# Performance work log

Measured on AMD Instinct MI355X. Metric: run time of the kernel, lower is better.

The kernel has to match this reference:

```python
import jax, jax.numpy as jnp
import numpy as np

B, T, D, DI, K, M, H, HD, L, VOCAB = 8, 512, 256, 512, 4, 2, 4, 64, 2, 272


def rmsnorm(x, w, eps=1e-6):
    return x * jax.lax.rsqrt(jnp.mean(x * x, axis=-1, keepdims=True) + eps) * w


def rotate_half(x):
    x1, x2 = x[..., ::2], x[..., 1::2]
    return jnp.stack([-x2, x1], axis=-1).reshape(x.shape)


def causal_conv(x, w, b):
    # x: [B,T,C], w: [C,K] depthwise causal conv, then silu
    y = jax.lax.conv_general_dilated(
        x.transpose(0, 2, 1), w[:, None, :],
        window_strides=(1,), padding=[(K - 1, 0)],
        feature_group_count=x.shape[-1])
    return jax.nn.silu(y.transpose(0, 2, 1) + b)


def delta_memory(x, Wv, Wg, Wb, Wa, A_log, dt_bias, Wblend, Wout):
    # x: [B,T,D]; per-timestep delta-rule fast-weight update with decay + key rotation
    Bv, Tn, Dm = x.shape
    vals = (x @ Wv).reshape(Bv, Tn, M, H, HD)
    gate = jax.nn.sigmoid(x @ Wg)                                   # [B,T,H]
    beta = jax.nn.sigmoid(jnp.einsum('btd,mdh->btmh', x, Wb))       # [B,T,M,H]
    alpha = jnp.einsum('btd,mdh->btmh', x, Wa) + dt_bias            # [B,T,M,H]
    decay = jnp.exp(-jnp.exp(A_log)[None, None] * jax.nn.softplus(alpha))
    blend = jax.nn.softmax((x @ Wblend).reshape(Bv, Tn, H, M), axis=-1)
    rk0 = x.reshape(Bv, Tn, H, HD)
    rk0 = rk0 / jnp.maximum(jnp.linalg.norm(rk0, axis=-1, keepdims=True), 1e-12)
    rks = [rk0]
    for _ in range(M - 1):
        rks.append(rotate_half(rks[-1]))
    rks = jnp.stack(rks, axis=2)                                    # [B,T,M,H,d]
    wks = jnp.pad(rks[:, :-1], ((0, 0), (1, 0), (0, 0), (0, 0), (0, 0)))  # shifted keys

    def step(S, inp):
        v, wk, rk, bt, dc, bl, g = inp
        S = S * dc[..., None, None]                                  # [B,M,H,d,d]
        pred = jnp.einsum('bmhdk,bmhd->bmhk', S, wk)
        err = (v - pred) * bt[..., None]
        S = S + wk[..., None] * err[..., None, :]                    # outer-product write
        read = jnp.einsum('bmhdk,bmhd->bmhk', S, rk)
        o = jnp.einsum('bhm,bmhk->bhk', bl, read) * g[..., None]
        return S, o

    tf = lambda a: jnp.moveaxis(a, 1, 0)
    xs = (tf(vals), tf(wks), tf(rks), tf(beta), tf(decay), tf(blend), tf(gate))
    S0 = jnp.zeros((Bv, M, H, HD, HD), x.dtype)
    _, o = jax.lax.scan(step, S0, xs)                                # [T,B,H,d]
    o = jnp.moveaxis(o, 0, 1).reshape(Bv, Tn, Dm)
    return x + o @ Wout


def setup_inputs():
    key = jax.random.key(0)
    ks = jax.random.split(key, 16)
    n = lambda k, shape, sc=0.02: jax.random.normal(k, shape, jnp.float32) * sc
    return {
        'ids': jax.random.randint(ks[0], (B, T), 0, VOCAB, jnp.int32),
        'emb': n(ks[1], (VOCAB, D)),
        'norm_w': jnp.ones((L, D), jnp.float32),
        'W_up': n(ks[2], (L, D, DI)),
        'W_gate': n(ks[3], (L, D, DI)),
        'W_down': n(ks[4], (L, DI, D)),
        'conv_w': n(ks[5], (L, DI, K), 0.1),
        'conv_b': jnp.zeros((L, DI), jnp.float32),
        'Wv': n(ks[6], (L, D, M * D)),
        'Wg': n(ks[7], (L, D, H)),
        'Wb': n(ks[8], (L, M, D, H)),
        'Wa': n(ks[9], (L, M, D, H)),
        'A_log': n(ks[10], (L, M, H), 0.5),
        'dt_bias': n(ks[11], (L, M, H), 0.5),
        'Wblend': n(ks[12], (L, D, H * M)),
        'Wout': n(ks[13], (L, D, D)),
        'final_norm_w': jnp.ones((D,), jnp.float32),
    }


def reference(ids, emb, norm_w, W_up, W_gate, W_down, conv_w, conv_b,
              Wv, Wg, Wb, Wa, A_log, dt_bias, Wblend, Wout, final_norm_w):
    x = emb[ids]
    for l in range(L):
        nx = rmsnorm(x, norm_w[l])
        h = causal_conv(nx @ W_up[l], conv_w[l], conv_b[l])
        out = (jax.nn.silu(nx @ W_gate[l]) * h) @ W_down[l]
        out = delta_memory(out, Wv[l], Wg[l], Wb[l], Wa[l],
                           A_log[l], dt_bias[l], Wblend[l], Wout[l])
        x = x + out
    return rmsnorm(x, final_norm_w) @ emb.T  # tied head
```

## Files before the change

kernel.cpp:

```cpp
#include <hip/hip_runtime.h>
#include <math.h>

#define BB 8
#define TT 512
#define DD 256
#define DIM 512
#define KW 4
#define MM 2
#define HH 4
#define HDIM 64
#define LL 2
#define VV 272

typedef __attribute__((ext_vector_type(8))) short bf16x8;
typedef __attribute__((ext_vector_type(4))) float f32x4;

__device__ __forceinline__ float sigf(float x){ return 1.f/(1.f+__expf(-x)); }
__device__ __forceinline__ float siluf(float x){ return x/(1.f+__expf(-x)); }

__device__ __forceinline__ unsigned short f2bf(float f){
  unsigned int u = __float_as_uint(f);
  unsigned int r = (u + 0x7FFFu + ((u >> 16) & 1u)) >> 16;
  return (unsigned short)r;
}
__device__ __forceinline__ float bf2f(unsigned short s){
  return __uint_as_float(((unsigned int)s) << 16);
}

__device__ __forceinline__ float xor1_add(float x){
  int y = __builtin_amdgcn_update_dpp(0, __float_as_int(x), 0xB1, 0xF, 0xF, true);
  return x + __int_as_float(y);
}
__device__ __forceinline__ float xor2_add(float x){
  int y = __builtin_amdgcn_update_dpp(0, __float_as_int(x), 0x4E, 0xF, 0xF, true);
  return x + __int_as_float(y);
}
__device__ __forceinline__ float ror4_add(float x){
  int y = __builtin_amdgcn_update_dpp(0, __float_as_int(x), 0x124, 0xF, 0xF, true);
  return x + __int_as_float(y);
}
__device__ __forceinline__ float ror8_add(float x){
  int y = __builtin_amdgcn_update_dpp(0, __float_as_int(x), 0x128, 0xF, 0xF, true);
  return x + __int_as_float(y);
}

__device__ __forceinline__ void gl_lds16(const void* g, void* l){
  __builtin_amdgcn_global_load_lds(
      (const __attribute__((address_space(1))) unsigned int*)g,
      (__attribute__((address_space(3))) unsigned int*)l,
      16, 0, 0);
}

#define LWB 589824
__global__ void k_cvt(const float* __restrict__ Wup, const float* __restrict__ Wgate,
                      const float* __restrict__ Wdown, const float* __restrict__ Wv,
                      const float* __restrict__ Wout, const float* __restrict__ emb,
                      unsigned short* __restrict__ wbf){
  int idx = blockIdx.x*256 + threadIdx.x;
  if (idx >= 2*LWB + VV*DD) return;
  float v;
  if (idx < 2*LWB){
    int l = (idx >= LWB) ? 1 : 0;
    int local = idx - l*LWB;
    if (local < 131072){ int n = local>>8, k = local&255;
      v = Wup[(size_t)l*131072 + k*DIM + n]; }
    else if (local < 262144){ local -= 131072; int n = local>>8, k = local&255;
      v = Wgate[(size_t)l*131072 + k*DIM + n]; }
    else if (local < 393216){ local -= 262144; int n = local>>9, k = local&511;
      v = Wdown[(size_t)l*131072 + k*DD + n]; }
    else if (local < 524288){ local -= 393216; int n = local>>8, k = local&255;
      v = Wv[(size_t)l*131072 + k*DIM + n]; }
    else { local -= 524288; int n = local>>8, k = local&255;
      v = Wout[(size_t)l*65536 + k*DD + n]; }
  } else {
    v = emb[idx - 2*LWB];
  }
  wbf[idx] = f2bf(v);
}

__global__ void k_embed(const int* __restrict__ ids, const float* __restrict__ emb,
                        float* __restrict__ x){
  int row = blockIdx.x;
  int d = threadIdx.x;
  x[row*DD + d] = emb[ids[row]*DD + d];
}

__global__ void k_rmsnorm(const float* __restrict__ in, const float* __restrict__ w,
                          unsigned short* __restrict__ out){
  int row = blockIdx.x;
  int l = threadIdx.x;
  float4 v = *(const float4*)&in[row*DD + l*4];
  float ss = v.x*v.x + v.y*v.y + v.z*v.z + v.w*v.w;
  #pragma unroll
  for (int o = 32; o > 0; o >>= 1) ss += __shfl_xor(ss, o, 64);
  float sc = rsqrtf(ss*(1.f/DD) + 1e-6f);
  float4 wv = *(const float4*)&w[l*4];
  ushort4 r;
  r.x = f2bf(v.x*sc*wv.x); r.y = f2bf(v.y*sc*wv.y);
  r.z = f2bf(v.z*sc*wv.z); r.w = f2bf(v.w*sc*wv.w);
  *(ushort4*)&out[row*DD + l*4] = r;
}

template<int MODE>
__global__ void __launch_bounds__(256) k_gemm64(const unsigned short* __restrict__ A,
                                                const unsigned short* __restrict__ Bt,
                                                float* __restrict__ Cf,
                                                unsigned short* __restrict__ Cb,
                                                int N, int K){
  __shared__ unsigned short as[64][72];
  __shared__ unsigned short bs[64][72];
  const int tid = threadIdx.x;
  const int w = tid >> 6, l = tid & 63;
  const int m0 = blockIdx.y*64, n0 = blockIdx.x*64;
  const int ar = tid >> 2, ac = (tid & 3)*16;
  f32x4 acc[4] = {};
  for (int k0 = 0; k0 < K; k0 += 64){
    { const bf16x8* src = (const bf16x8*)&A[(size_t)(m0+ar)*K + k0 + ac];
      *(bf16x8*)&as[ar][ac]   = src[0];
      *(bf16x8*)&as[ar][ac+8] = src[1];
    }
    { int n = n0 + ar;
      bf16x8 z; z = (bf16x8)(short)0;
      bf16x8 b0 = z, b1 = z;
      if (n < N){
        const bf16x8* src = (const bf16x8*)&Bt[(size_t)n*K + k0 + ac];
        b0 = src[0]; b1 = src[1];
      }
      *(bf16x8*)&bs[ar][ac]   = b0;
      *(bf16x8*)&bs[ar][ac+8] = b1;
    }
    __syncthreads();
    const int mr = w*16 + (l & 15);
    const int kb = (l >> 4)*8;
    #pragma unroll
    for (int kc2 = 0; kc2 < 2; ++kc2){
      bf16x8 af = *(const bf16x8*)&as[mr][kc2*32 + kb];
      #pragma unroll
      for (int nt = 0; nt < 4; ++nt){
        bf16x8 bfr = *(const bf16x8*)&bs[nt*16 + (l & 15)][kc2*32 + kb];
        acc[nt] = __builtin_amdgcn_mfma_f32_16x16x32_bf16(af, bfr, acc[nt], 0, 0, 0);
      }
    }
    __syncthreads();
  }
  #pragma unroll
  for (int nt = 0; nt < 4; ++nt){
    int col = n0 + nt*16 + (l & 15);
    if (col < N){
      #pragma unroll
      for (int r = 0; r < 4; ++r){
        int row = m0 + w*16 + (l >> 4)*4 + r;
        if (MODE == 0 || MODE == 2) Cf[(size_t)row*N + col] = acc[nt][r];
        if (MODE == 1 || MODE == 2) Cb[(size_t)row*N + col] = f2bf(acc[nt][r]);
      }
    }
  }
}

template<int MODE>
__global__ void __launch_bounds__(256) k_gemm128(const unsigned short* __restrict__ A,
                                                 const unsigned short* __restrict__ Bt,
                                                 float* __restrict__ Cf,
                                                 unsigned short* __restrict__ Cb,
                                                 int N, int K){
  __shared__ unsigned short as[128][72];
  __shared__ unsigned short bs[64][72];
  const int tid = threadIdx.x;
  const int w = tid >> 6, l = tid & 63;
  const int m0 = blockIdx.y*128, n0 = blockIdx.x*64;
  const int ar = tid >> 1, ac = (tid & 1)*32;
  const int br = tid >> 2, bc = (tid & 3)*16;
  f32x4 acc[2][4] = {};
  for (int k0 = 0; k0 < K; k0 += 64){
    { const bf16x8* src = (const bf16x8*)&A[(size_t)(m0+ar)*K + k0 + ac];
      *(bf16x8*)&as[ar][ac]    = src[0];
      *(bf16x8*)&as[ar][ac+8]  = src[1];
      *(bf16x8*)&as[ar][ac+16] = src[2];
      *(bf16x8*)&as[ar][ac+24] = src[3];
    }
    { int n = n0 + br;
      bf16x8 z; z = (bf16x8)(short)0;
      bf16x8 b0 = z, b1 = z;
      if (n < N){
        const bf16x8* s = (const bf16x8*)&Bt[(size_t)n*K + k0 + bc];
        b0 = s[0]; b1 = s[1];
      }
      *(bf16x8*)&bs[br][bc]   = b0;
      *(bf16x8*)&bs[br][bc+8] = b1;
    }
    __syncthreads();
    const int lr = l & 15, kb = (l >> 4)*8;
    #pragma unroll
    for (int kc2 = 0; kc2 < 2; ++kc2){
      bf16x8 af0 = *(const bf16x8*)&as[w*32 + lr][kc2*32 + kb];
      bf16x8 af1 = *(const bf16x8*)&as[w*32 + 16 + lr][kc2*32 + kb];
      #pragma unroll
      for (int nt = 0; nt < 4; ++nt){
        bf16x8 bfr = *(const bf16x8*)&bs[nt*16 + lr][kc2*32 + kb];
        acc[0][nt] = __builtin_amdgcn_mfma_f32_16x16x32_bf16(af0, bfr, acc[0][nt], 0, 0, 0);
        acc[1][nt] = __builtin_amdgcn_mfma_f32_16x16x32_bf16(af1, bfr, acc[1][nt], 0, 0, 0);
      }
    }
    __syncthreads();
  }
  const int lr = l & 15;
  #pragma unroll
  for (int mt = 0; mt < 2; ++mt){
    #pragma unroll
    for (int nt = 0; nt < 4; ++nt){
      int col = n0 + nt*16 + lr;
      if (col < N){
        #pragma unroll
        for (int r = 0; r < 4; ++r){
          int row = m0 + w*32 + mt*16 + (l >> 4)*4 + r;
          if (MODE == 0 || MODE == 2) Cf[(size_t)row*N + col] = acc[mt][nt][r];
          if (MODE == 1 || MODE == 2) Cb[(size_t)row*N + col] = f2bf(acc[mt][nt][r]);
        }
      }
    }
  }
}

__global__ void __launch_bounds__(256) k_gemm_up(const unsigned short* __restrict__ A,
                                                 const unsigned short* __restrict__ But,
                                                 const unsigned short* __restrict__ Bgt,
                                                 unsigned short* __restrict__ Cu,
                                                 unsigned short* __restrict__ Cg){
  __shared__ unsigned short as[128][72];
  __shared__ unsigned short bu[64][72];
  __shared__ unsigned short bg[64][72];
  const int tid = threadIdx.x;
  const int w = tid >> 6, l = tid & 63;
  const int m0 = blockIdx.y*128, n0 = blockIdx.x*64;
  const int ar = tid >> 1, ac = (tid & 1)*32;
  const int br = tid >> 2, bc = (tid & 3)*16;
  f32x4 accu[2][4] = {}; f32x4 accg[2][4] = {};
  for (int k0 = 0; k0 < DD; k0 += 64){
    { const bf16x8* src = (const bf16x8*)&A[(size_t)(m0+ar)*DD + k0 + ac];
      *(bf16x8*)&as[ar][ac]    = src[0];
      *(bf16x8*)&as[ar][ac+8]  = src[1];
      *(bf16x8*)&as[ar][ac+16] = src[2];
      *(bf16x8*)&as[ar][ac+24] = src[3];
    }
    { const bf16x8* s0 = (const bf16x8*)&But[(size_t)(n0+br)*DD + k0 + bc];
      *(bf16x8*)&bu[br][bc]   = s0[0];
      *(bf16x8*)&bu[br][bc+8] = s0[1];
      const bf16x8* s1 = (const bf16x8*)&Bgt[(size_t)(n0+br)*DD + k0 + bc];
      *(bf16x8*)&bg[br][bc]   = s1[0];
      *(bf16x8*)&bg[br][bc+8] = s1[1];
    }
    __syncthreads();
    const int lr = l & 15, kb = (l >> 4)*8;
    #pragma unroll
    for (int kc2 = 0; kc2 < 2; ++kc2){
      bf16x8 af0 = *(const bf16x8*)&as[w*32 + lr][kc2*32 + kb];
      bf16x8 af1 = *(const bf16x8*)&as[w*32 + 16 + lr][kc2*32 + kb];
      #pragma unroll
      for (int nt = 0; nt < 4; ++nt){
        bf16x8 b0 = *(const bf16x8*)&bu[nt*16 + lr][kc2*32 + kb];
        accu[0][nt] = __builtin_amdgcn_mfma_f32_16x16x32_bf16(af0, b0, accu[0][nt], 0, 0, 0);
        accu[1][nt] = __builtin_amdgcn_mfma_f32_16x16x32_bf16(af1, b0, accu[1][nt], 0, 0, 0);
        bf16x8 b1 = *(const bf16x8*)&bg[nt*16 + lr][kc2*32 + kb];
        accg[0][nt] = __builtin_amdgcn_mfma_f32_16x16x32_bf16(af0, b1, accg[0][nt], 0, 0, 0);
        accg[1][nt] = __builtin_amdgcn_mfma_f32_16x16x32_bf16(af1, b1, accg[1][nt], 0, 0, 0);
      }
    }
    __syncthreads();
  }
  const int lr = l & 15;
  #pragma unroll
  for (int mt = 0; mt < 2; ++mt){
    #pragma unroll
    for (int nt = 0; nt < 4; ++nt){
      int col = n0 + nt*16 + lr;
      #pragma unroll
      for (int r = 0; r < 4; ++r){
        int row = m0 + w*32 + mt*16 + (l >> 4)*4 + r;
        Cu[(size_t)row*DIM + col] = f2bf(accu[mt][nt][r]);
        Cg[(size_t)row*DIM + col] = f2bf(accg[mt][nt][r]);
      }
    }
  }
}

__global__ void __launch_bounds__(256) k_gemm_wout(const float* __restrict__ p0,
                                                   const float* __restrict__ p1,
                                                   const unsigned short* __restrict__ Bt,
                                                   const float* __restrict__ y,
                                                   float* __restrict__ x){
  __shared__ unsigned short as[64][72];
  __shared__ unsigned short bs[64][72];
  const int tid = threadIdx.x;
  const int w = tid >> 6, l = tid & 63;
  const int m0 = blockIdx.y*64, n0 = blockIdx.x*64;
  const int ar = tid >> 2, ac = (tid & 3)*16;
  f32x4 acc[4] = {};
  for (int k0 = 0; k0 < DD; k0 += 64){
    #pragma unroll
    for (int j = 0; j < 4; ++j){
      size_t off = (size_t)(m0+ar)*DD + k0 + ac + j*4;
      float4 a = *(const float4*)&p0[off];
      float4 b = *(const float4*)&p1[off];
      a.x += b.x; a.y += b.y; a.z += b.z; a.w += b.w;
      ushort4 u = make_ushort4(f2bf(a.x), f2bf(a.y), f2bf(a.z), f2bf(a.w));
      *(ushort4*)&as[ar][ac + j*4] = u;
    }
    { const bf16x8* src = (const bf16x8*)&Bt[(size_t)(n0+ar)*DD + k0 + ac];
      *(bf16x8*)&bs[ar][ac]   = src[0];
      *(bf16x8*)&bs[ar][ac+8] = src[1];
    }
    __syncthreads();
    const int mr = w*16 + (l & 15);
    const int kb = (l >> 4)*8;
    #pragma unroll
    for (int kc2 = 0; kc2 < 2; ++kc2){
      bf16x8 af = *(const bf16x8*)&as[mr][kc2*32 + kb];
      #pragma unroll
      for (int nt = 0; nt < 4; ++nt){
        bf16x8 bfr = *(const bf16x8*)&bs[nt*16 + (l & 15)][kc2*32 + kb];
        acc[nt] = __builtin_amdgcn_mfma_f32_16x16x32_bf16(af, bfr, acc[nt], 0, 0, 0);
      }
    }
    __syncthreads();
  }
  #pragma unroll
  for (int nt = 0; nt < 4; ++nt){
    int col = n0 + nt*16 + (l & 15);
    #pragma unroll
    for (int r = 0; r < 4; ++r){
      int row = m0 + w*16 + (l >> 4)*4 + r;
      size_t off = (size_t)row*DD + col;
      x[off] = x[off] + y[off] + acc[nt][r];
    }
  }
}

__global__ void k_conv(const unsigned short* __restrict__ u,
                       const unsigned short* __restrict__ g,
                       const float* __restrict__ cw, const float* __restrict__ cb,
                       unsigned short* __restrict__ hh){
  int i8 = blockIdx.x*256 + threadIdx.x;
  int cg = i8 & 63;
  int bt = i8 >> 6;
  int t  = bt & (TT-1);
  int c0 = cg*8;
  float acc[8];
  { float4 b0 = *(const float4*)&cb[c0];
    float4 b1 = *(const float4*)&cb[c0+4];
    acc[0]=b0.x; acc[1]=b0.y; acc[2]=b0.z; acc[3]=b0.w;
    acc[4]=b1.x; acc[5]=b1.y; acc[6]=b1.z; acc[7]=b1.w; }
  float wts[8][4];
  #pragma unroll
  for (int i = 0; i < 8; ++i) *(float4*)&wts[i][0] = *(const float4*)&cw[(c0+i)*KW];
  #pragma unroll
  for (int j = 0; j < KW; ++j){
    int dt_ = j - (KW-1);
    if (t + dt_ >= 0){
      bf16x8 uv = *(const bf16x8*)&u[(size_t)(bt + dt_)*DIM + c0];
      #pragma unroll
      for (int i = 0; i < 8; ++i)
        acc[i] = fmaf(bf2f((unsigned short)uv[i]), wts[i][j], acc[i]);
    }
  }
  bf16x8 gv = *(const bf16x8*)&g[(size_t)bt*DIM + c0];
  bf16x8 o;
  #pragma unroll
  for (int i = 0; i < 8; ++i){
    float h = siluf(acc[i]);
    o[i] = (short)f2bf(siluf(bf2f((unsigned short)gv[i])) * h);
  }
  *(bf16x8*)&hh[(size_t)bt*DIM + c0] = o;
}

__global__ void __launch_bounds__(256) k_fused(const float* __restrict__ y,
    const float* __restrict__ Wg, const float* __restrict__ Wb,
    const float* __restrict__ Wa, const float* __restrict__ Wbl,
    const float* __restrict__ A_log, const float* __restrict__ dtb,
    float* __restrict__ rkb, float* __restrict__ scal){
  __shared__ float s_y[4][260];
  __shared__ float s_p[4][32];
  const int wv = threadIdx.x >> 6, l = threadIdx.x & 63;
  const int row = blockIdx.x*4 + wv;

  float4 yv = *(const float4*)&y[(size_t)row*DD + l*4];
  *(float4*)&s_y[wv][l*4] = yv;

  float ss = yv.x*yv.x + yv.y*yv.y + yv.z*yv.z + yv.w*yv.w;
  ss = xor1_add(ss); ss = xor2_add(ss);
  ss = ror4_add(ss); ss = ror8_add(ss);
  float inv = 1.f / fmaxf(sqrtf(ss), 1e-12f);
  float4 rv; rv.x = yv.x*inv; rv.y = yv.y*inv; rv.z = yv.z*inv; rv.w = yv.w*inv;
  *(float4*)&rkb[(size_t)row*DD + l*4] = rv;

  __syncthreads();

  const int j = (l < 28) ? l : 27;
  const float* wp; int stride;
  if (j < 4){ wp = Wg + j; stride = HH; }
  else if (j < 12){ int m=(j-4)>>2, h=(j-4)&3; wp = Wb + (size_t)m*DD*HH + h; stride = HH; }
  else if (j < 20){ int m=(j-12)>>2, h=(j-12)&3; wp = Wa + (size_t)m*DD*HH + h; stride = HH; }
  else { wp = Wbl + (j-20); stride = HH*MM; }
  float a0=0.f,a1=0.f,a2=0.f,a3=0.f;
  #pragma unroll 4
  for (int k = 0; k < DD; k += 4){
    a0 = fmaf(s_y[wv][k+0], wp[(k+0)*stride], a0);
    a1 = fmaf(s_y[wv][k+1], wp[(k+1)*stride], a1);
    a2 = fmaf(s_y[wv][k+2], wp[(k+2)*stride], a2);
    a3 = fmaf(s_y[wv][k+3], wp[(k+3)*stride], a3);
  }
  if (l < 28) s_p[wv][l] = (a0+a1)+(a2+a3);

  __syncthreads();

  if (l < 8){
    int m = l >> 2, h = l & 3;
    float gs  = sigf(s_p[wv][h]);
    float btv = sigf(s_p[wv][4 + m*4 + h]);
    float sp  = s_p[wv][12 + m*4 + h] + dtb[m*HH + h];
    sp = (sp > 15.f) ? sp : log1pf(__expf(sp));
    float dc  = __expf(-__expf(A_log[m*HH + h]) * sp);
    float l0 = s_p[wv][20 + h*2], l1 = s_p[wv][20 + h*2 + 1];
    float mx = fmaxf(l0, l1);
    float e0 = __expf(l0-mx), e1 = __expf(l1-mx);
    float bl = (m ? e1 : e0) / (e0 + e1);
    float4 o; o.x = dc; o.y = btv; o.z = bl*gs; o.w = 0.f;
    *(float4*)&scal[((size_t)row*MM + m)*(HH*4) + h*4] = o;
  }
}


#define SSTEP(T_, WK, RK, PF, VB, SB) { \
  const float dc = SB.x, btv = SB.y, blg = SB.z; \
  const float v = VB; \
  { const int tn_ = ((T_)+2 < 64) ? (T_)+2 : 63; \
    PF = *(const float4*)&s_rk[p][tn_][dbase]; \
    VB = bf2f(s_v[p][tn_][vidx]); \
    SB = *(const float4*)&s_sc[p][tn_][0]; } \
  const float err = (v - dc*rrc)*btv; \
  float rr0=0.f, rr1=0.f; \
  { const float4 rp = WK; const float4 rc = RK; \
    float w0,w1,w2,w3,c0,c1,c2,c3; \
    if (ROT == 0){ w0=rp.x; w1=rp.y; w2=rp.z; w3=rp.w; c0=rc.x; c1=rc.y; c2=rc.z; c3=rc.w; } \
    else { w0=-rp.y; w1=rp.x; w2=-rp.w; w3=rp.z; c0=-rc.y; c1=rc.x; c2=-rc.w; c3=rc.z; } \
    S[0] = fmaf(S[0], dc, w0*err); rr0 = fmaf(S[0], c0, rr0); \
    S[1] = fmaf(S[1], dc, w1*err); rr1 = fmaf(S[1], c1, rr1); \
    S[2] = fmaf(S[2], dc, w2*err); rr0 = fmaf(S[2], c2, rr0); \
    S[3] = fmaf(S[3], dc, w3*err); rr1 = fmaf(S[3], c3, rr1); } \
  float rr = rr0 + rr1; \
  rr = xor1_add(rr); rr = xor2_add(rr); rr = ror4_add(rr); rr = ror8_add(rr); \
  rrc = rr; \
  if (seg == 0) part[(size_t)(rowchunk + (T_))*DD + h*HDIM + kq4*4 + klocal] = blg*rr; \
}

template<int ROT>
__device__ __forceinline__ void scan_body(int b, int h, int kq4, int l,
    const unsigned short* __restrict__ vals, const float* __restrict__ rkb,
    const float* __restrict__ scal, float* __restrict__ part,
    float (*s_rk)[64][64], unsigned short (*s_v)[64][8], float (*s_sc)[64][4])
{
  const int seg = l & 15, klocal = l >> 4;
  const int dbase = seg*4;
  const int vidx = (kq4 & 1)*4 + klocal;
  const int kq8 = kq4 >> 1;
  const int rowbase = b*TT;

  float S[4];
  #pragma unroll
  for (int j = 0; j < 4; ++j) S[j] = 0.f;
  const float4 Z = make_float4(0.f,0.f,0.f,0.f);
  float4 rb0 = Z, rb1 = Z, rb2 = Z, rb3 = Z;
  float vb0 = 0.f, vb1 = 0.f;
  float4 sb0 = Z, sb1 = Z;
  float rrc = 0.f;

  auto stage = [&](int c, int pbuf){
    const int r0 = rowbase + c*64;
    #pragma unroll
    for (int i = 0; i < 16; ++i){
      const float* g = rkb + (size_t)(r0 + i*4 + (l>>4))*DD + h*HDIM + (l&15)*4;
      gl_lds16(g, &s_rk[pbuf][i*4][0]);
    }
    { const unsigned short* g = vals + ((size_t)(r0 + l)*MM + ROT)*DD + h*HDIM + kq8*8;
      gl_lds16(g, &s_v[pbuf][0][0]); }
    { const float* g = scal + ((size_t)(r0 + l)*MM + ROT)*(HH*4) + h*4;
      gl_lds16(g, &s_sc[pbuf][0][0]); }
  };

  stage(0, 0);
  for (int c = 0; c < TT/64; ++c){
    const int p = c & 1;
    __syncthreads();
    if (c + 1 < TT/64) stage(c+1, p^1);
    rb0 = *(const float4*)&s_rk[p][0][dbase];
    rb1 = *(const float4*)&s_rk[p][1][dbase];
    vb0 = bf2f(s_v[p][0][vidx]); vb1 = bf2f(s_v[p][1][vidx]);
    sb0 = *(const float4*)&s_sc[p][0][0]; sb1 = *(const float4*)&s_sc[p][1][0];
    const int rowchunk = rowbase + c*64;
    for (int tt = 0; tt < 64; tt += 4){
      SSTEP(tt+0, rb3, rb0, rb2, vb0, sb0)
      SSTEP(tt+1, rb0, rb1, rb3, vb1, sb1)
      SSTEP(tt+2, rb1, rb2, rb0, vb0, sb0)
      SSTEP(tt+3, rb2, rb3, rb1, vb1, sb1)
    }
  }
}

__global__ void __launch_bounds__(64) k_scan(const unsigned short* __restrict__ vals,
                                             const float* __restrict__ rkb,
                                             const float* __restrict__ scal,
                                             float* __restrict__ partials){
  __shared__ float s_rk[2][64][64];
  __shared__ unsigned short s_v[2][64][8];
  __shared__ float s_sc[2][64][4];
  const int bi = blockIdx.x;
  const int kq4 = bi & 15;
  const int m  = (bi >> 4) & 1;
  const int h  = (bi >> 5) & 3;
  const int b  = bi >> 7;
  float* part = partials + (size_t)m*(BB*TT*DD);
  if (m == 0) scan_body<0>(b, h, kq4, threadIdx.x, vals, rkb, scal, part, s_rk, s_v, s_sc);
  else        scan_body<1>(b, h, kq4, threadIdx.x, vals, rkb, scal, part, s_rk, s_v, s_sc);
}

extern "C" void kernel_launch(void* const* d_in, const int* in_sizes, int n_in,
                              void* d_out, int out_size, void* d_ws, size_t ws_size,
                              hipStream_t stream){
  const int*   ids   = (const int*)d_in[0];
  const float* emb   = (const float*)d_in[1];
  const float* normw = (const float*)d_in[2];
  const float* Wup   = (const float*)d_in[3];
  const float* Wgate = (const float*)d_in[4];
  const float* Wdown = (const float*)d_in[5];
  const float* convw = (const float*)d_in[6];
  const float* convb = (const float*)d_in[7];
  const float* Wv    = (const float*)d_in[8];
  const float* Wg    = (const float*)d_in[9];
  const float* Wb    = (const float*)d_in[10];
  const float* Wa    = (const float*)d_in[11];
  const float* A_log = (const float*)d_in[12];
  const float* dtb   = (const float*)d_in[13];
  const float* Wbl   = (const float*)d_in[14];
  const float* Wout  = (const float*)d_in[15];
  const float* fnw   = (const float*)d_in[16];
  float* out = (float*)d_out;

  const int ROWS = BB*TT;
  const size_t MEG = 1u << 20;
  float* ws   = (float*)d_ws;
  float* x    = ws;
  unsigned short* nyb = (unsigned short*)(x + MEG);
  float* big1 = x + MEG + MEG/2;
  float* big2 = big1 + 2*MEG;
  float* y    = big2 + 2*MEG;
  float* rkb  = y    + MEG;
  float* scal = rkb  + MEG;
  unsigned short* wbf = (unsigned short*)(scal + (1u<<17));

  unsigned short* ub  = (unsigned short*)big1;
  unsigned short* gb  = (unsigned short*)(big1 + MEG);
  unsigned short* valsb = ub;

  { int total = 2*LWB + VV*DD;
    k_cvt<<<(total + 255)/256, 256, 0, stream>>>(Wup, Wgate, Wdown, Wv, Wout, emb, wbf); }

  k_embed<<<ROWS, DD, 0, stream>>>(ids, emb, x);

  for (int l = 0; l < LL; ++l){
    unsigned short* wl = wbf + (size_t)l*LWB;
    unsigned short* upT   = wl;
    unsigned short* gateT = wl + 131072;
    unsigned short* downT = wl + 262144;
    unsigned short* wvT   = wl + 393216;
    unsigned short* woutT = wl + 524288;

    k_rmsnorm<<<ROWS, 64, 0, stream>>>(x, normw + l*DD, nyb);
    k_gemm_up<<<dim3(DIM/64, ROWS/128), 256, 0, stream>>>(nyb, upT, gateT, ub, gb);
    k_conv<<<(ROWS*DIM/8)/256, 256, 0, stream>>>(ub, gb, convw + l*DIM*KW, convb + l*DIM, gb);
    k_gemm64<2><<<dim3(DD/64, ROWS/64), 256, 0, stream>>>(gb, downT, y, nyb, DD, DIM);
    k_gemm128<1><<<dim3(DIM/64, ROWS/128), 256, 0, stream>>>(nyb, wvT, nullptr, valsb, DIM, DD);
    k_fused<<<ROWS/4, 256, 0, stream>>>(y, Wg + l*DD*HH, Wb + (size_t)l*MM*DD*HH,
                                        Wa + (size_t)l*MM*DD*HH, Wbl + l*DD*HH*MM,
                                        A_log + l*MM*HH, dtb + l*MM*HH, rkb, scal);
    k_scan<<<BB*HH*MM*16, 64, 0, stream>>>(valsb, rkb, scal, big2);
    k_gemm_wout<<<dim3(DD/64, ROWS/64), 256, 0, stream>>>(big2, big2 + MEG, woutT, y, x);
  }

  unsigned short* embT = wbf + 2*LWB;
  k_rmsnorm<<<ROWS, 64, 0, stream>>>(x, fnw, nyb);
  k_gemm64<0><<<dim3((VV+63)/64, ROWS/64), 256, 0, stream>>>(nyb, embT, out, nullptr, VV, DD);
}
```

Before: 289.8 us.

## Split delta-rule scan across twice as many blocks with bf16 rotated keys

The scan kernel now gives each lane two state elements instead of four, with 32 lanes per key column and two columns per wave. It launches twice as many single-wave blocks to shorten the serial per-step dependency chain and raise parallelism. The normalized keys are stored and staged in bf16, which halves their global and LDS traffic. Costs are an extra cross-lane shuffle per step, more redundant staging of keys across blocks, and reduced key precision.

```diff
diff --git a/kernel.cpp b/kernel.cpp
--- a/kernel.cpp
+++ b/kernel.cpp
@@ -376,7 +376,7 @@
     const float* __restrict__ Wg, const float* __restrict__ Wb,
     const float* __restrict__ Wa, const float* __restrict__ Wbl,
     const float* __restrict__ A_log, const float* __restrict__ dtb,
-    float* __restrict__ rkb, float* __restrict__ scal){
+    unsigned short* __restrict__ rkb, float* __restrict__ scal){
   __shared__ float s_y[4][260];
   __shared__ float s_p[4][32];
   const int wv = threadIdx.x >> 6, l = threadIdx.x & 63;
@@ -389,8 +389,10 @@
   ss = xor1_add(ss); ss = xor2_add(ss);
   ss = ror4_add(ss); ss = ror8_add(ss);
   float inv = 1.f / fmaxf(sqrtf(ss), 1e-12f);
-  float4 rv; rv.x = yv.x*inv; rv.y = yv.y*inv; rv.z = yv.z*inv; rv.w = yv.w*inv;
-  *(float4*)&rkb[(size_t)row*DD + l*4] = rv;
+  ushort4 rv;
+  rv.x = f2bf(yv.x*inv); rv.y = f2bf(yv.y*inv);
+  rv.z = f2bf(yv.z*inv); rv.w = f2bf(yv.w*inv);
+  *(ushort4*)&rkb[(size_t)row*DD + l*4] = rv;
 
   __syncthreads();
 
@@ -433,54 +435,50 @@
   const float dc = SB.x, btv = SB.y, blg = SB.z; \
   const float v = VB; \
   { const int tn_ = ((T_)+2 < 64) ? (T_)+2 : 63; \
-    PF = *(const float4*)&s_rk[p][tn_][dbase]; \
+    ushort2 rw = *(const ushort2*)&s_rk[p][tn_][dbase]; \
+    PF.x = bf2f(rw.x); PF.y = bf2f(rw.y); \
     VB = bf2f(s_v[p][tn_][vidx]); \
     SB = *(const float4*)&s_sc[p][tn_][0]; } \
   const float err = (v - dc*rrc)*btv; \
-  float rr0=0.f, rr1=0.f; \
-  { const float4 rp = WK; const float4 rc = RK; \
-    float w0,w1,w2,w3,c0,c1,c2,c3; \
-    if (ROT == 0){ w0=rp.x; w1=rp.y; w2=rp.z; w3=rp.w; c0=rc.x; c1=rc.y; c2=rc.z; c3=rc.w; } \
-    else { w0=-rp.y; w1=rp.x; w2=-rp.w; w3=rp.z; c0=-rc.y; c1=rc.x; c2=-rc.w; c3=rc.z; } \
-    S[0] = fmaf(S[0], dc, w0*err); rr0 = fmaf(S[0], c0, rr0); \
-    S[1] = fmaf(S[1], dc, w1*err); rr1 = fmaf(S[1], c1, rr1); \
-    S[2] = fmaf(S[2], dc, w2*err); rr0 = fmaf(S[2], c2, rr0); \
-    S[3] = fmaf(S[3], dc, w3*err); rr1 = fmaf(S[3], c3, rr1); } \
-  float rr = rr0 + rr1; \
+  float w0, w1, c0, c1; \
+  if (ROT == 0){ w0 = WK.x; w1 = WK.y; c0 = RK.x; c1 = RK.y; } \
+  else { w0 = -WK.y; w1 = WK.x; c0 = -RK.y; c1 = RK.x; } \
+  S0 = fmaf(S0, dc, w0*err); \
+  S1 = fmaf(S1, dc, w1*err); \
+  float rr = S0*c0; rr = fmaf(S1, c1, rr); \
   rr = xor1_add(rr); rr = xor2_add(rr); rr = ror4_add(rr); rr = ror8_add(rr); \
+  rr += __shfl_xor(rr, 16, 64); \
   rrc = rr; \
-  if (seg == 0) part[(size_t)(rowchunk + (T_))*DD + h*HDIM + kq4*4 + klocal] = blg*rr; \
+  if (seg == 0) part[(size_t)(rowchunk + (T_))*DD + h*HDIM + kq2*2 + klocal] = blg*rr; \
 }
 
 template<int ROT>
-__device__ __forceinline__ void scan_body(int b, int h, int kq4, int l,
-    const unsigned short* __restrict__ vals, const float* __restrict__ rkb,
+__device__ __forceinline__ void scan_body(int b, int h, int kq2, int l,
+    const unsigned short* __restrict__ vals, const unsigned short* __restrict__ rkb,
     const float* __restrict__ scal, float* __restrict__ part,
-    float (*s_rk)[64][64], unsigned short (*s_v)[64][8], float (*s_sc)[64][4])
+    unsigned short (*s_rk)[64][64], unsigned short (*s_v)[64][8], float (*s_sc)[64][4])
 {
-  const int seg = l & 15, klocal = l >> 4;
-  const int dbase = seg*4;
-  const int vidx = (kq4 & 1)*4 + klocal;
-  const int kq8 = kq4 >> 1;
+  const int seg = l & 31, klocal = l >> 5;
+  const int dbase = seg*2;
+  const int vidx = (kq2 & 3)*2 + klocal;
+  const int kq16 = kq2 >> 2;
   const int rowbase = b*TT;
 
-  float S[4];
-  #pragma unroll
-  for (int j = 0; j < 4; ++j) S[j] = 0.f;
+  float S0 = 0.f, S1 = 0.f;
+  float2 rb0 = make_float2(0.f,0.f), rb1 = rb0, rb2 = rb0, rb3 = rb0;
+  float vb0 = 0.f, vb1 = 0.f;
   const float4 Z = make_float4(0.f,0.f,0.f,0.f);
-  float4 rb0 = Z, rb1 = Z, rb2 = Z, rb3 = Z;
-  float vb0 = 0.f, vb1 = 0.f;
   float4 sb0 = Z, sb1 = Z;
   float rrc = 0.f;
 
   auto stage = [&](int c, int pbuf){
     const int r0 = rowbase + c*64;
     #pragma unroll
-    for (int i = 0; i < 16; ++i){
-      const float* g = rkb + (size_t)(r0 + i*4 + (l>>4))*DD + h*HDIM + (l&15)*4;
-      gl_lds16(g, &s_rk[pbuf][i*4][0]);
-    }
-    { const unsigned short* g = vals + ((size_t)(r0 + l)*MM + ROT)*DD + h*HDIM + kq8*8;
+    for (int i = 0; i < 8; ++i){
+      const unsigned short* g = rkb + (size_t)(r0 + i*8 + (l>>3))*DD + h*HDIM + (l&7)*8;
+      gl_lds16(g, &s_rk[pbuf][i*8][0]);
+    }
+    { const unsigned short* g = vals + ((size_t)(r0 + l)*MM + ROT)*DD + h*HDIM + kq16*8;
       gl_lds16(g, &s_v[pbuf][0][0]); }
     { const float* g = scal + ((size_t)(r0 + l)*MM + ROT)*(HH*4) + h*4;
       gl_lds16(g, &s_sc[pbuf][0][0]); }
@@ -491,8 +489,10 @@
     const int p = c & 1;
     __syncthreads();
     if (c + 1 < TT/64) stage(c+1, p^1);
-    rb0 = *(const float4*)&s_rk[p][0][dbase];
-    rb1 = *(const float4*)&s_rk[p][1][dbase];
+    { ushort2 r0v = *(const ushort2*)&s_rk[p][0][dbase];
+      rb0.x = bf2f(r0v.x); rb0.y = bf2f(r0v.y);
+      ushort2 r1v = *(const ushort2*)&s_rk[p][1][dbase];
+      rb1.x = bf2f(r1v.x); rb1.y = bf2f(r1v.y); }
     vb0 = bf2f(s_v[p][0][vidx]); vb1 = bf2f(s_v[p][1][vidx]);
     sb0 = *(const float4*)&s_sc[p][0][0]; sb1 = *(const float4*)&s_sc[p][1][0];
     const int rowchunk = rowbase + c*64;
@@ -506,20 +506,20 @@
 }
 
 __global__ void __launch_bounds__(64) k_scan(const unsigned short* __restrict__ vals,
-                                             const float* __restrict__ rkb,
+                                             const unsigned short* __restrict__ rkb,
                                              const float* __restrict__ scal,
                                              float* __restrict__ partials){
-  __shared__ float s_rk[2][64][64];
+  __shared__ unsigned short s_rk[2][64][64];
   __shared__ unsigned short s_v[2][64][8];
   __shared__ float s_sc[2][64][4];
   const int bi = blockIdx.x;
-  const int kq4 = bi & 15;
-  const int m  = (bi >> 4) & 1;
-  const int h  = (bi >> 5) & 3;
-  const int b  = bi >> 7;
+  const int kq2 = bi & 31;
+  const int m  = (bi >> 5) & 1;
+  const int h  = (bi >> 6) & 3;
+  const int b  = bi >> 8;
   float* part = partials + (size_t)m*(BB*TT*DD);
-  if (m == 0) scan_body<0>(b, h, kq4, threadIdx.x, vals, rkb, scal, part, s_rk, s_v, s_sc);
-  else        scan_body<1>(b, h, kq4, threadIdx.x, vals, rkb, scal, part, s_rk, s_v, s_sc);
+  if (m == 0) scan_body<0>(b, h, kq2, threadIdx.x, vals, rkb, scal, part, s_rk, s_v, s_sc);
+  else        scan_body<1>(b, h, kq2, threadIdx.x, vals, rkb, scal, part, s_rk, s_v, s_sc);
 }
 
 extern "C" void kernel_launch(void* const* d_in, const int* in_sizes, int n_in,
@@ -552,8 +552,8 @@
   float* big1 = x + MEG + MEG/2;
   float* big2 = big1 + 2*MEG;
   float* y    = big2 + 2*MEG;
-  float* rkb  = y    + MEG;
-  float* scal = rkb  + MEG;
+  unsigned short* rkb = (unsigned short*)(y + MEG);
+  float* scal = y + MEG + MEG/2;
   unsigned short* wbf = (unsigned short*)(scal + (1u<<17));
 
   unsigned short* ub  = (unsigned short*)big1;
@@ -581,7 +581,7 @@
     k_fused<<<ROWS/4, 256, 0, stream>>>(y, Wg + l*DD*HH, Wb + (size_t)l*MM*DD*HH,
                                         Wa + (size_t)l*MM*DD*HH, Wbl + l*DD*HH*MM,
                                         A_log + l*MM*HH, dtb + l*MM*HH, rkb, scal);
-    k_scan<<<BB*HH*MM*16, 64, 0, stream>>>(valsb, rkb, scal, big2);
+    k_scan<<<BB*HH*MM*32, 64, 0, stream>>>(valsb, rkb, scal, big2);
     k_gemm_wout<<<dim3(DD/64, ROWS/64), 256, 0, stream>>>(big2, big2 + MEG, woutT, y, x);
   }
 
```

New measurement: 311.6 us. 1.08x slower.
